# Kernel tuning notes

Measured on AMD Instinct MI355X. Metric: run time of the kernel, lower is better.

The kernel has to match this reference:

```python
import jax, jax.numpy as jnp
import numpy as np

B, T, D, NH, V, L = 2, 1024, 1024, 16, 32000, 4  # L = blocks * layers_per_block
HD = D // NH
FF = 4 * D


def rmsnorm(x, gamma, beta):
    # matches RMSNorm: mean of squares over last dim (tp pmean is identity on 1 device)
    ms = jnp.mean(jnp.square(x), axis=-1, keepdims=True)
    return (x / jnp.sqrt(ms + 1e-6)) * gamma + beta


def setup_inputs() -> dict:
    key = jax.random.key(0)
    ks = jax.random.split(key, 16)
    s = 0.02
    inp = {
        "tokens": jax.random.randint(ks[0], (B, T), 0, V, dtype=jnp.int32),
        "emb_W": jax.random.normal(ks[1], (V, D), jnp.float32) * s,
        "pos_W": jax.random.normal(ks[2], (T, D), jnp.float32) * s,
        "g1": jnp.ones((L, D), jnp.float32),
        "be1": jnp.zeros((L, D), jnp.float32),
        "Wqkv": jax.random.normal(ks[3], (L, D, 3 * D), jnp.float32) * s,
        "bqkv": jnp.zeros((L, 3 * D), jnp.float32),
        "Wo": jax.random.normal(ks[4], (L, D, D), jnp.float32) * s,
        "bo": jnp.zeros((L, D), jnp.float32),
        "g2": jnp.ones((L, D), jnp.float32),
        "be2": jnp.zeros((L, D), jnp.float32),
        "Wf1": jax.random.normal(ks[5], (L, D, FF), jnp.float32) * s,
        "bf1": jnp.zeros((L, FF), jnp.float32),
        "Wf2": jax.random.normal(ks[6], (L, FF, D), jnp.float32) * s,
        "bf2": jnp.zeros((L, D), jnp.float32),
        "gf": jnp.ones((D,), jnp.float32),
        "bef": jnp.zeros((D,), jnp.float32),
    }
    return inp


def _forward(tokens, emb_W, pos_W, g1, be1, Wqkv, bqkv, Wo, bo, g2, be2,
             Wf1, bf1, Wf2, bf2, gf, bef):
    x = emb_W[tokens] + pos_W[jnp.arange(T)]  # [B, T, D]
    causal = jnp.tril(jnp.ones((T, T), dtype=bool))
    scale = HD ** -0.5
    for i in range(L):
        # attention sub-block
        h = rmsnorm(x, g1[i], be1[i])
        qkv = h @ Wqkv[i] + bqkv[i]
        q, k, v = jnp.split(qkv, 3, axis=-1)
        q = q.reshape(B, T, NH, HD).transpose(0, 2, 1, 3)  # B nh T d
        k = k.reshape(B, T, NH, HD).transpose(0, 2, 1, 3)
        v = v.reshape(B, T, NH, HD).transpose(0, 2, 1, 3)
        att = jnp.einsum('bhqd,bhkd->bhqk', q, k) * scale
        att = jnp.where(causal, att, -jnp.inf)
        att = jax.nn.softmax(att, axis=-1)
        o = jnp.einsum('bhqk,bhkd->bhqd', att, v)
        o = o.transpose(0, 2, 1, 3).reshape(B, T, D)
        x = x + (o @ Wo[i] + bo[i])
        # FFN sub-block (selu, dropout off since train=False)
        h = rmsnorm(x, g2[i], be2[i])
        f = jax.nn.selu(h @ Wf1[i] + bf1[i]) @ Wf2[i] + bf2[i]
        x = x + f
    # tied output head: final RMSNorm then embedding.attend
    x = rmsnorm(x, gf, bef)
    logits = jnp.einsum('btd,vd->btv', x, emb_W)
    return logits


def reference(tokens, emb_W, pos_W, g1, be1, Wqkv, bqkv, Wo, bo, g2, be2,
              Wf1, bf1, Wf2, bf2, gf, bef):
    return _forward(tokens, emb_W, pos_W, g1, be1, Wqkv, bqkv, Wo, bo,
                    g2, be2, Wf1, bf1, Wf2, bf2, gf, bef)
```

## Files before the change

### kernel.cpp

```cpp
#include <hip/hip_runtime.h>

typedef unsigned short u16;
typedef __attribute__((ext_vector_type(8))) short bf16x8;
typedef __attribute__((ext_vector_type(4))) float f32x4;

#define DD 1024
#define TT 1024
#define NHH 16
#define VV 32000
#define FFF 4096
#define LL 4
#define MM 2048
#define TD3 3072

__device__ __forceinline__ u16 f2bfu(float f) {
  unsigned int x = __builtin_bit_cast(unsigned int, f);
  return (u16)((x + 0x7FFFu + ((x >> 16) & 1u)) >> 16);
}

__device__ __forceinline__ void gl16(const u16* g, u16* l) {
  __builtin_amdgcn_global_load_lds((const __attribute__((address_space(1))) void*)g,
                                   (__attribute__((address_space(3))) void*)l, 16, 0, 0);
}

template <int N>
__device__ __forceinline__ void vwait() {
  if constexpr (N == 0) asm volatile("s_waitcnt vmcnt(0)" ::: "memory");
  else if constexpr (N == 4) asm volatile("s_waitcnt vmcnt(4)" ::: "memory");
  else asm volatile("s_waitcnt vmcnt(8)" ::: "memory");
}

__global__ void transpose_cvt_k(const float* __restrict__ in, u16* __restrict__ out,
                                int K, int N) {
  const size_t mat = (size_t)K * N;
  in += (size_t)blockIdx.z * mat;
  out += (size_t)blockIdx.z * mat;
  __shared__ float tile[32][33];
  const int n0 = blockIdx.x << 5, k0 = blockIdx.y << 5;
  const int tx = threadIdx.x, ty = threadIdx.y;
#pragma unroll
  for (int i = 0; i < 32; i += 8) tile[ty + i][tx] = in[(size_t)(k0 + ty + i) * N + n0 + tx];
  __syncthreads();
#pragma unroll
  for (int i = 0; i < 32; i += 8)
    out[(size_t)(n0 + ty + i) * K + k0 + tx] = f2bfu(tile[tx][ty + i]);
}

__global__ void cvt_bf16_k(const float* __restrict__ in, u16* __restrict__ out, long n4) {
  const long i = (long)blockIdx.x * blockDim.x + threadIdx.x;
  if (i >= n4) return;
  const float4 v = ((const float4*)in)[i];
  ushort4 o;
  o.x = f2bfu(v.x); o.y = f2bfu(v.y); o.z = f2bfu(v.z); o.w = f2bfu(v.w);
  ((ushort4*)out)[i] = o;
}

__global__ void embed_k(const int* __restrict__ tok, const float* __restrict__ emb,
                        const float* __restrict__ pos, float* __restrict__ x) {
  const int m = blockIdx.x, tid = threadIdx.x;
  const int t = m & (TT - 1);
  const int id = tok[m];
  const float4 e = ((const float4*)(emb + (size_t)id * DD))[tid];
  const float4 p = ((const float4*)(pos + (size_t)t * DD))[tid];
  float4 r;
  r.x = e.x + p.x; r.y = e.y + p.y; r.z = e.z + p.z; r.w = e.w + p.w;
  ((float4*)(x + (size_t)m * DD))[tid] = r;
}

__global__ void rmsnorm_k(const float* __restrict__ x, const float* __restrict__ g,
                          const float* __restrict__ be, u16* __restrict__ out) {
  const int row = blockIdx.x, tid = threadIdx.x;
  const float4 xv = ((const float4*)(x + (size_t)row * DD))[tid];
  float ss = xv.x * xv.x + xv.y * xv.y + xv.z * xv.z + xv.w * xv.w;
#pragma unroll
  for (int o = 32; o; o >>= 1) ss += __shfl_xor(ss, o);
  __shared__ float sm[4];
  if ((tid & 63) == 0) sm[tid >> 6] = ss;
  __syncthreads();
  const float tot = sm[0] + sm[1] + sm[2] + sm[3];
  const float rs = rsqrtf(tot * (1.f / DD) + 1e-6f);
  const float4 gv = ((const float4*)g)[tid];
  const float4 bv = ((const float4*)be)[tid];
  ushort4 o4;
  o4.x = f2bfu(xv.x * rs * gv.x + bv.x);
  o4.y = f2bfu(xv.y * rs * gv.y + bv.y);
  o4.z = f2bfu(xv.z * rs * gv.z + bv.z);
  o4.w = f2bfu(xv.w * rs * gv.w + bv.w);
  ((ushort4*)(out + (size_t)row * DD))[tid] = o4;
}

template <int NP>
__global__ void addres_rms_k(float* __restrict__ x, const float* __restrict__ pp,
                             const float* __restrict__ bias, const float* __restrict__ g,
                             const float* __restrict__ be, u16* __restrict__ out) {
  const int row = blockIdx.x, tid = threadIdx.x;
  const size_t base = (size_t)row * (DD / 4) + tid;
  float4 s = ((float4*)x)[base];
  const float4 bv = ((const float4*)bias)[tid];
  s.x += bv.x; s.y += bv.y; s.z += bv.z; s.w += bv.w;
#pragma unroll
  for (int p = 0; p < NP; ++p) {
    const float4 pv = ((const float4*)pp)[(size_t)p * (MM * DD / 4) + base];
    s.x += pv.x; s.y += pv.y; s.z += pv.z; s.w += pv.w;
  }
  ((float4*)x)[base] = s;
  float ss = s.x * s.x + s.y * s.y + s.z * s.z + s.w * s.w;
#pragma unroll
  for (int o = 32; o; o >>= 1) ss += __shfl_xor(ss, o);
  __shared__ float sm[4];
  if ((tid & 63) == 0) sm[tid >> 6] = ss;
  __syncthreads();
  const float tot = sm[0] + sm[1] + sm[2] + sm[3];
  const float rs = rsqrtf(tot * (1.f / DD) + 1e-6f);
  const float4 gv = ((const float4*)g)[tid];
  const float4 bev = ((const float4*)be)[tid];
  ushort4 o4;
  o4.x = f2bfu(s.x * rs * gv.x + bev.x);
  o4.y = f2bfu(s.y * rs * gv.y + bev.y);
  o4.z = f2bfu(s.z * rs * gv.z + bev.z);
  o4.w = f2bfu(s.w * rs * gv.w + bev.w);
  ((ushort4*)(out + (size_t)row * DD))[tid] = o4;
}

__global__ void pack_vt_k(const u16* __restrict__ qkv, u16* __restrict__ Vt) {
  const int z = blockIdx.x;
  const int t0 = blockIdx.y << 6;
  const int b = z >> 4, h = z & 15;
  __shared__ u16 tile[64][72];
  const int tid = threadIdx.x;
  for (int c = tid; c < 512; c += 256) {
    const int t = c >> 3, d8 = (c & 7) << 3;
    union { uint4 u; u16 s[8]; } tmp;
    tmp.u = *(const uint4*)(qkv + (long)(b * TT + t0 + t) * TD3 + 2 * DD + h * 64 + d8);
#pragma unroll
    for (int j = 0; j < 8; ++j) tile[d8 + j][t] = tmp.s[j];
  }
  __syncthreads();
  for (int c = tid; c < 512; c += 256) {
    const int d = c >> 3, t8 = (c & 7) << 3;
    *(uint4*)(Vt + ((long)z * 64 + d) * TT + t0 + t8) = *(const uint4*)&tile[d][t8];
  }
}

__global__ __launch_bounds__(256) void flash_k(const u16* __restrict__ qkv,
                                               const u16* __restrict__ Vt,
                                               u16* __restrict__ o) {
  const int z = blockIdx.x;
  const int pair = blockIdx.y;
  const int b = z >> 4, h = z & 15;
  const int tid = threadIdx.x;
  const int lane = tid & 63;
  const int w = tid >> 6;

  __shared__ u16 Qs[64 * 64];
  __shared__ u16 Ks[128 * 64];
  __shared__ u16 Vs[64 * 128];
  __shared__ u16 Ps[64 * 128];

  const u16* qbase = qkv + (size_t)b * TT * TD3;
  const int kcb = (lane >> 4) << 4;

  for (int half = 0; half < 2; ++half) {
    const int qa = half ? (15 - pair) : pair;
    const int q0 = qa << 6;
    const int nkt = (qa >> 1) + 1;

#pragma unroll
    for (int c = 0; c < 2; ++c) {
      const int rbase = c * 32 + w * 8;
      const int row = rbase + (lane >> 3);
      const u16* src = qbase + (long)(q0 + row) * TD3 + h * 64 +
                       ((((lane & 7) << 4) ^ ((row & 7) << 4)) >> 1);
      gl16(src, &Qs[rbase * 64]);
    }

    float m_r[4], l_r[4];
    f32x4 oacc[4];
#pragma unroll
    for (int r = 0; r < 4; ++r) { m_r[r] = -1e30f; l_r[r] = 0.f; }
#pragma unroll
    for (int nd = 0; nd < 4; ++nd) oacc[nd] = (f32x4){0.f, 0.f, 0.f, 0.f};

    for (int kt = 0; kt < nkt; ++kt) {
      const int t0 = kt << 7;
#pragma unroll
      for (int c = 0; c < 4; ++c) {
        const int rbase = c * 32 + w * 8;
        const int row = rbase + (lane >> 3);
        const u16* src = qbase + (long)(t0 + row) * TD3 + DD + h * 64 +
                         ((((lane & 7) << 4) ^ ((row & 7) << 4)) >> 1);
        gl16(src, &Ks[rbase * 64]);
      }
#pragma unroll
      for (int c = 0; c < 4; ++c) {
        const int rbase = c * 16 + w * 4;
        const int d = rbase + (lane >> 4);
        const u16* src = Vt + ((long)(z * 64 + d)) * TT + t0 +
                         ((((lane & 15) << 4) ^ ((d & 7) << 4)) >> 1);
        gl16(src, &Vs[rbase * 128]);
      }
      __syncthreads();

      f32x4 sacc[8];
#pragma unroll
      for (int ni = 0; ni < 8; ++ni) sacc[ni] = (f32x4){0.f, 0.f, 0.f, 0.f};
      const int qrow = (w << 4) + (lane & 15);
#pragma unroll
      for (int ks = 0; ks < 2; ++ks) {
        const bf16x8 aq = *(const bf16x8*)&Qs[qrow * 64 + (((ks * 64 + kcb) ^ ((qrow & 7) << 4)) >> 1)];
#pragma unroll
        for (int ni = 0; ni < 8; ++ni) {
          const int key = (lane & 15) + (ni << 4);
          const bf16x8 bk = *(const bf16x8*)&Ks[key * 64 + (((ks * 64 + kcb) ^ ((key & 7) << 4)) >> 1)];
          sacc[ni] = __builtin_amdgcn_mfma_f32_16x16x32_bf16(aq, bk, sacc[ni], 0, 0, 0);
        }
      }

      float mx[4] = {-1e30f, -1e30f, -1e30f, -1e30f};
      const bool diag = (kt == nkt - 1);
#pragma unroll
      for (int ni = 0; ni < 8; ++ni)
#pragma unroll
        for (int r = 0; r < 4; ++r) {
          float v = sacc[ni][r] * 0.125f;
          if (diag) {
            const int key = t0 + (lane & 15) + (ni << 4);
            const int qq = q0 + (w << 4) + ((lane >> 4) << 2) + r;
            if (key > qq) v = -1e30f;
          }
          sacc[ni][r] = v;
          mx[r] = fmaxf(mx[r], v);
        }
#pragma unroll
      for (int st = 1; st < 16; st <<= 1)
#pragma unroll
        for (int r = 0; r < 4; ++r) mx[r] = fmaxf(mx[r], __shfl_xor(mx[r], st));
      float sc[4], sum[4];
#pragma unroll
      for (int r = 0; r < 4; ++r) {
        const float mn = fmaxf(m_r[r], mx[r]);
        sc[r] = __expf(m_r[r] - mn);
        m_r[r] = mn;
        sum[r] = 0.f;
      }
#pragma unroll
      for (int ni = 0; ni < 8; ++ni)
#pragma unroll
        for (int r = 0; r < 4; ++r) {
          const float e = __expf(sacc[ni][r] - m_r[r]);
          sum[r] += e;
          const int prow = (w << 4) + ((lane >> 4) << 2) + r;
          const int pcol = (lane & 15) + (ni << 4);
          Ps[prow * 128 + (((pcol << 1) ^ ((prow & 7) << 4)) >> 1)] = f2bfu(e);
        }
#pragma unroll
      for (int st = 1; st < 16; st <<= 1)
#pragma unroll
        for (int r = 0; r < 4; ++r) sum[r] += __shfl_xor(sum[r], st);
#pragma unroll
      for (int r = 0; r < 4; ++r) l_r[r] = l_r[r] * sc[r] + sum[r];
#pragma unroll
      for (int nd = 0; nd < 4; ++nd)
#pragma unroll
        for (int r = 0; r < 4; ++r) oacc[nd][r] *= sc[r];

#pragma unroll
      for (int ks2 = 0; ks2 < 4; ++ks2) {
        const int prow = (w << 4) + (lane & 15);
        const bf16x8 pa = *(const bf16x8*)&Ps[prow * 128 + (((ks2 * 64 + kcb) ^ ((prow & 7) << 4)) >> 1)];
#pragma unroll
        for (int nd = 0; nd < 4; ++nd) {
          const int dd2 = (lane & 15) + (nd << 4);
          const bf16x8 vb = *(const bf16x8*)&Vs[dd2 * 128 + (((ks2 * 64 + kcb) ^ ((dd2 & 7) << 4)) >> 1)];
          oacc[nd] = __builtin_amdgcn_mfma_f32_16x16x32_bf16(pa, vb, oacc[nd], 0, 0, 0);
        }
      }
      __syncthreads();
    }

    float inv[4];
#pragma unroll
    for (int r = 0; r < 4; ++r) inv[r] = 1.f / l_r[r];
#pragma unroll
    for (int nd = 0; nd < 4; ++nd)
#pragma unroll
      for (int r = 0; r < 4; ++r) {
        const int row = q0 + (w << 4) + ((lane >> 4) << 2) + r;
        const int col = (h << 6) + (lane & 15) + (nd << 4);
        o[(long)(b * TT + row) * DD + col] = f2bfu(oacc[nd][r] * inv[r]);
      }
  }
}

enum { EPI_BF16 = 0, EPI_BF16_BIAS = 1, EPI_SELU = 2, EPI_F32 = 3, EPI_RESID = 4 };

template <int EPI>
__global__ __launch_bounds__(256) void gemm_bt(
    const u16* __restrict__ A, long az1, long az2, int lda,
    const u16* __restrict__ Bt, long bz1, long bz2, int ldb,
    void* __restrict__ C, long cz1, long cz2, int ldc,
    const float* __restrict__ bias, int Nvalid, int K) {
  const int z = blockIdx.z;
  A += (long)(z >> 4) * az1 + (long)(z & 15) * az2;
  Bt += (long)(z >> 4) * bz1 + (long)(z & 15) * bz2;
  const long coff = (long)(z >> 4) * cz1 + (long)(z & 15) * cz2;

  __shared__ u16 ldsA[2][128 * 32];
  __shared__ u16 ldsB[2][128 * 32];

  const int tid = threadIdx.x;
  const int lane = tid & 63;
  const int wave = tid >> 6;
  const int wr = wave >> 1, wc = wave & 1;
  const int m0 = blockIdx.x << 7, n0 = blockIdx.y << 7;

  f32x4 acc[4][4];
#pragma unroll
  for (int i = 0; i < 4; ++i)
#pragma unroll
    for (int j = 0; j < 4; ++j) acc[i][j] = (f32x4){0.f, 0.f, 0.f, 0.f};

  auto STAGE = [&](int buf, int kt) {
    const int k0 = kt << 5;
#pragma unroll
    for (int p = 0; p < 2; ++p) {
      const int c = tid + (p << 8);
      const int row = c >> 2, col = (c & 3) << 3;
      gl16(A + (long)(m0 + row) * lda + k0 + col, &ldsA[buf][c << 3]);
      gl16(Bt + (long)(n0 + row) * ldb + k0 + col, &ldsB[buf][c << 3]);
    }
  };

  const int nk = K >> 5;
  STAGE(0, 0);
  __syncthreads();
  int cur = 0;
  for (int kt = 0; kt < nk; ++kt) {
    if (kt + 1 < nk) STAGE(cur ^ 1, kt + 1);
    const int rb = lane & 15;
    const int kc = (lane >> 4) << 3;
    bf16x8 af[4], bfr[4];
#pragma unroll
    for (int mi = 0; mi < 4; ++mi)
      af[mi] = *(const bf16x8*)&ldsA[cur][(((wr << 6) + (mi << 4) + rb) << 5) + kc];
#pragma unroll
    for (int ni = 0; ni < 4; ++ni)
      bfr[ni] = *(const bf16x8*)&ldsB[cur][(((wc << 6) + (ni << 4) + rb) << 5) + kc];
#pragma unroll
    for (int mi = 0; mi < 4; ++mi)
#pragma unroll
      for (int ni = 0; ni < 4; ++ni)
        acc[mi][ni] = __builtin_amdgcn_mfma_f32_16x16x32_bf16(af[mi], bfr[ni], acc[mi][ni], 0, 0, 0);
    __syncthreads();
    cur ^= 1;
  }

  const int row0 = m0 + (wr << 6) + ((lane >> 4) << 2);
  const int col0 = n0 + (wc << 6) + (lane & 15);
#pragma unroll
  for (int ni = 0; ni < 4; ++ni) {
    const int col = col0 + (ni << 4);
    if (col >= Nvalid) continue;
    float bv = 0.f;
    if (EPI == EPI_BF16_BIAS || EPI == EPI_SELU || EPI == EPI_RESID) bv = bias[col];
#pragma unroll
    for (int mi = 0; mi < 4; ++mi) {
#pragma unroll
      for (int r = 0; r < 4; ++r) {
        const int row = row0 + (mi << 4) + r;
        const long idx = coff + (long)row * ldc + col;
        float v = acc[mi][ni][r] + bv;
        if (EPI == EPI_SELU)
          v = v > 0.f ? 1.0507009873554805f * v : 1.7580993408473766f * (__expf(v) - 1.f);
        if (EPI == EPI_BF16 || EPI == EPI_BF16_BIAS || EPI == EPI_SELU)
          ((u16*)C)[idx] = f2bfu(v);
        else if (EPI == EPI_F32)
          ((float*)C)[idx] = v;
        else
          ((float*)C)[idx] += v;
      }
    }
  }
}

template <int EPI, int KDIM>
__global__ __launch_bounds__(512) void gemm256_k(
    const u16* __restrict__ A, int lda,
    const u16* __restrict__ Bt, int ldb,
    void* __restrict__ C, int ldc,
    const float* __restrict__ bias, int mm) {
  extern __shared__ u16 smem[];
  u16* SA = smem;
  u16* SB = smem + 24576;

  const int nwg = gridDim.x;
  const int q = nwg >> 3, r = nwg & 7;
  const int xcd = blockIdx.x & 7, loc = blockIdx.x >> 3;
  const int wg = (xcd < r) ? (xcd * (q + 1) + loc) : (r * (q + 1) + (xcd - r) * q + loc);
  const int m0 = (wg % mm) << 8;
  const int n0 = (wg / mm) << 8;

  const int tid = threadIdx.x;
  const int lane = tid & 63;
  const int w = tid >> 6;
  const int wr = w >> 2, wc = w & 3;
  const int l = lane & 15, kq = lane >> 4;

  f32x4 acc[8][4];
#pragma unroll
  for (int i = 0; i < 8; ++i)
#pragma unroll
    for (int j = 0; j < 4; ++j) acc[i][j] = (f32x4){0.f, 0.f, 0.f, 0.f};

  auto STAGE = [&](int p, int kt) {
    u16* la = SA + (p << 13);
    u16* lb = SB + (p << 13);
    const int k0 = kt << 5;
#pragma unroll
    for (int hh = 0; hh < 2; ++hh) {
      const int c = tid + (hh << 9);
      const int r2 = c >> 3, sp = c & 7;
      const int s = sp ^ (r2 & 7);
      const int row = r2 + ((s >> 2) << 7);
      const int col = k0 + ((s & 3) << 3);
      gl16(A + (size_t)(m0 + row) * lda + col, la + (c << 3));
      gl16(Bt + (size_t)(n0 + row) * ldb + col, lb + (c << 3));
    }
  };

  constexpr int NK = KDIM >> 5;
  STAGE(0, 0);
  STAGE(1, 1);
  STAGE(2, 2);

  int buf = 0;
#pragma unroll 1
  for (int t = 0; t < NK; ++t) {
    if (t + 2 < NK) vwait<8>();
    else if (t + 1 < NK) vwait<4>();
    else vwait<0>();
    __builtin_amdgcn_s_barrier();
    __builtin_amdgcn_sched_barrier(0);

    const u16* a = SA + (buf << 13);
    const u16* b = SB + (buf << 13);
    auto rdA = [&](int mi) -> bf16x8 {
      const int row = (wr << 7) + (mi << 4) + l;
      const int r2 = row & 127;
      const int sp = (((row >> 7) << 2) + kq) ^ (r2 & 7);
      return *(const bf16x8*)&a[(r2 << 6) + (sp << 3)];
    };
    auto rdB = [&](int ni) -> bf16x8 {
      const int row = (wc << 6) + (ni << 4) + l;
      const int r2 = row & 127;
      const int sp = (((row >> 7) << 2) + kq) ^ (r2 & 7);
      return *(const bf16x8*)&b[(r2 << 6) + (sp << 3)];
    };

    bf16x8 bfr[4], afA[2], afB[2];
    bfr[0] = rdB(0); bfr[1] = rdB(1); bfr[2] = rdB(2); bfr[3] = rdB(3);
    afA[0] = rdA(0); afA[1] = rdA(1);
    __builtin_amdgcn_sched_barrier(0);
    afB[0] = rdA(2); afB[1] = rdA(3);
    __builtin_amdgcn_sched_barrier(0);

    __builtin_amdgcn_s_setprio(1);
#pragma unroll
    for (int ni = 0; ni < 4; ++ni) {
      acc[0][ni] = __builtin_amdgcn_mfma_f32_16x16x32_bf16(afA[0], bfr[ni], acc[0][ni], 0, 0, 0);
      acc[1][ni] = __builtin_amdgcn_mfma_f32_16x16x32_bf16(afA[1], bfr[ni], acc[1][ni], 0, 0, 0);
    }
    __builtin_amdgcn_s_setprio(0);
    __builtin_amdgcn_sched_barrier(0);
    afA[0] = rdA(4); afA[1] = rdA(5);
    __builtin_amdgcn_sched_barrier(0);
    __builtin_amdgcn_s_setprio(1);
#pragma unroll
    for (int ni = 0; ni < 4; ++ni) {
      acc[2][ni] = __builtin_amdgcn_mfma_f32_16x16x32_bf16(afB[0], bfr[ni], acc[2][ni], 0, 0, 0);
      acc[3][ni] = __builtin_amdgcn_mfma_f32_16x16x32_bf16(afB[1], bfr[ni], acc[3][ni], 0, 0, 0);
    }
    __builtin_amdgcn_s_setprio(0);
    __builtin_amdgcn_sched_barrier(0);
    afB[0] = rdA(6); afB[1] = rdA(7);
    __builtin_amdgcn_sched_barrier(0);
    __builtin_amdgcn_s_setprio(1);
#pragma unroll
    for (int ni = 0; ni < 4; ++ni) {
      acc[4][ni] = __builtin_amdgcn_mfma_f32_16x16x32_bf16(afA[0], bfr[ni], acc[4][ni], 0, 0, 0);
      acc[5][ni] = __builtin_amdgcn_mfma_f32_16x16x32_bf16(afA[1], bfr[ni], acc[5][ni], 0, 0, 0);
    }
    __builtin_amdgcn_s_setprio(0);
    __builtin_amdgcn_sched_barrier(0);

    asm volatile("s_waitcnt lgkmcnt(0)" ::: "memory");
    __builtin_amdgcn_sched_barrier(0);
    __builtin_amdgcn_s_barrier();
    __builtin_amdgcn_sched_barrier(0);
    if (t + 3 < NK) STAGE(buf, t + 3);
    __builtin_amdgcn_sched_barrier(0);

    __builtin_amdgcn_s_setprio(1);
#pragma unroll
    for (int ni = 0; ni < 4; ++ni) {
      acc[6][ni] = __builtin_amdgcn_mfma_f32_16x16x32_bf16(afB[0], bfr[ni], acc[6][ni], 0, 0, 0);
      acc[7][ni] = __builtin_amdgcn_mfma_f32_16x16x32_bf16(afB[1], bfr[ni], acc[7][ni], 0, 0, 0);
    }
    __builtin_amdgcn_s_setprio(0);
    buf = (buf == 2) ? 0 : buf + 1;
  }

  const int row0 = m0 + (wr << 7) + ((lane >> 4) << 2);
  const int col0 = n0 + (wc << 6) + (lane & 15);
#pragma unroll
  for (int ni = 0; ni < 4; ++ni) {
    const int col = col0 + (ni << 4);
    float bv = 0.f;
    if (EPI == EPI_BF16_BIAS || EPI == EPI_SELU) bv = bias[col];
#pragma unroll
    for (int mi = 0; mi < 8; ++mi) {
#pragma unroll
      for (int r = 0; r < 4; ++r) {
        const int row = row0 + (mi << 4) + r;
        const long idx = (long)row * ldc + col;
        float v = acc[mi][ni][r] + bv;
        if (EPI == EPI_SELU)
          v = v > 0.f ? 1.0507009873554805f * v : 1.7580993408473766f * (__expf(v) - 1.f);
        if (EPI == EPI_BF16 || EPI == EPI_BF16_BIAS || EPI == EPI_SELU)
          ((u16*)C)[idx] = f2bfu(v);
        else
          ((float*)C)[idx] = v;
      }
    }
  }
}

extern "C" void kernel_launch(void* const* d_in, const int* in_sizes, int n_in,
                              void* d_out, int out_size, void* d_ws, size_t ws_size,
                              hipStream_t stream) {
  const int* tokens = (const int*)d_in[0];
  const float* emb_W = (const float*)d_in[1];
  const float* pos_W = (const float*)d_in[2];
  const float* g1 = (const float*)d_in[3];
  const float* be1 = (const float*)d_in[4];
  const float* Wqkv = (const float*)d_in[5];
  const float* bqkv = (const float*)d_in[6];
  const float* Wo = (const float*)d_in[7];
  const float* bo = (const float*)d_in[8];
  const float* g2 = (const float*)d_in[9];
  const float* be2 = (const float*)d_in[10];
  const float* Wf1 = (const float*)d_in[11];
  const float* bf1 = (const float*)d_in[12];
  const float* Wf2 = (const float*)d_in[13];
  const float* bf2 = (const float*)d_in[14];
  const float* gf = (const float*)d_in[15];
  const float* bef = (const float*)d_in[16];

  char* w = (char*)d_ws;
  auto alloc = [&](size_t bytes) {
    char* p = w;
    w += (bytes + 255) & ~(size_t)255;
    return p;
  };
  u16* WqkvT = (u16*)alloc((size_t)LL * TD3 * DD * 2);
  u16* WoT   = (u16*)alloc((size_t)LL * DD * DD * 2);
  u16* Wf1T  = (u16*)alloc((size_t)LL * FFF * DD * 2);
  u16* Wf2T  = (u16*)alloc((size_t)LL * DD * FFF * 2);
  u16* embB  = (u16*)alloc((size_t)VV * DD * 2);
  float* x   = (float*)alloc((size_t)MM * DD * 4);
  u16* h     = (u16*)alloc((size_t)MM * DD * 2);
  u16* qkv   = (u16*)alloc((size_t)MM * TD3 * 2);
  u16* Vt    = (u16*)alloc((size_t)32 * 64 * TT * 2);
  u16* o     = (u16*)alloc((size_t)MM * DD * 2);
  u16* h1    = (u16*)alloc((size_t)MM * FFF * 2);
  float* pp  = (float*)alloc((size_t)4 * MM * DD * 4);

  bool big =
      hipFuncSetAttribute((const void*)&gemm256_k<EPI_F32, 1024>,
                          hipFuncAttributeMaxDynamicSharedMemorySize, 98304) == hipSuccess;

  dim3 tb(32, 8);
  transpose_cvt_k<<<dim3(TD3 / 32, DD / 32, LL), tb, 0, stream>>>(Wqkv, WqkvT, DD, TD3);
  transpose_cvt_k<<<dim3(DD / 32, DD / 32, LL), tb, 0, stream>>>(Wo, WoT, DD, DD);
  transpose_cvt_k<<<dim3(FFF / 32, DD / 32, LL), tb, 0, stream>>>(Wf1, Wf1T, DD, FFF);
  transpose_cvt_k<<<dim3(DD / 32, FFF / 32, LL), tb, 0, stream>>>(Wf2, Wf2T, FFF, DD);
  cvt_bf16_k<<<(VV * DD / 4) / 256, 256, 0, stream>>>(emb_W, embB, (long)VV * DD / 4);
  embed_k<<<MM, 256, 0, stream>>>(tokens, emb_W, pos_W, x);
  rmsnorm_k<<<MM, 256, 0, stream>>>(x, g1, be1, h);

  for (int i = 0; i < LL; ++i) {
    gemm_bt<EPI_BF16_BIAS><<<dim3(16, 24, 1), 256, 0, stream>>>(
        h, 0, 0, DD, WqkvT + (size_t)i * TD3 * DD, 0, 0, DD,
        qkv, 0, 0, TD3, bqkv + i * TD3, TD3, DD);
    pack_vt_k<<<dim3(32, 16), 256, 0, stream>>>(qkv, Vt);
    flash_k<<<dim3(32, 8), 256, 0, stream>>>(qkv, Vt, o);
    gemm_bt<EPI_F32><<<dim3(16, 8, 2), 256, 0, stream>>>(
        o, 0, 512, DD, WoT + (size_t)i * DD * DD, 0, 512, DD,
        pp, 0, (long)MM * DD, DD, nullptr, DD, 512);
    addres_rms_k<2><<<MM, 256, 0, stream>>>(x, pp, bo + i * DD, g2 + i * DD, be2 + i * DD, h);
    gemm_bt<EPI_SELU><<<dim3(16, 32, 1), 256, 0, stream>>>(
        h, 0, 0, DD, Wf1T + (size_t)i * FFF * DD, 0, 0, DD,
        h1, 0, 0, FFF, bf1 + i * FFF, FFF, DD);
    gemm_bt<EPI_F32><<<dim3(16, 8, 4), 256, 0, stream>>>(
        h1, 0, 1024, FFF, Wf2T + (size_t)i * DD * FFF, 0, 1024, FFF,
        pp, 0, (long)MM * DD, DD, nullptr, DD, 1024);
    const bool last = (i == LL - 1);
    addres_rms_k<4><<<MM, 256, 0, stream>>>(
        x, pp, bf2 + i * DD,
        last ? gf : g1 + (i + 1) * DD, last ? bef : be1 + (i + 1) * DD, h);
  }

  if (big) {
    gemm256_k<EPI_F32, 1024><<<1000, 512, 98304, stream>>>(
        h, DD, embB, DD, (float*)d_out, VV, nullptr, 8);
  } else {
    gemm_bt<EPI_F32><<<dim3(16, 250, 1), 256, 0, stream>>>(
        h, 0, 0, DD, embB, 0, 0, DD,
        (float*)d_out, 0, 0, VV, nullptr, VV, DD);
  }
}
```

Measured before the change: 993.8 us.

## Add triple-buffered layer GEMM, restructure logits GEMM loop and LDS-staged epilogue

Result: slower. 1.064 ms (+7.1%).

```diff
diff --git a/kernel.cpp b/kernel.cpp
--- a/kernel.cpp
+++ b/kernel.cpp
@@ -383,12 +383,116 @@
   }
 }
 
-template <int EPI, int KDIM>
+template <int EPI>
+__global__ __launch_bounds__(256) void gemm_bt3(
+    const u16* __restrict__ A, long az1, long az2, int lda,
+    const u16* __restrict__ Bt, long bz1, long bz2, int ldb,
+    void* __restrict__ C, long cz1, long cz2, int ldc,
+    const float* __restrict__ bias, int Nvalid, int K) {
+  const int z = blockIdx.z;
+  A += (long)(z >> 4) * az1 + (long)(z & 15) * az2;
+  Bt += (long)(z >> 4) * bz1 + (long)(z & 15) * bz2;
+  const long coff = (long)(z >> 4) * cz1 + (long)(z & 15) * cz2;
+
+  __shared__ u16 ldsA[3][128 * 32];
+  __shared__ u16 ldsB[3][128 * 32];
+
+  const int tid = threadIdx.x;
+  const int lane = tid & 63;
+  const int wave = tid >> 6;
+  const int wr = wave >> 1, wc = wave & 1;
+  const int m0 = blockIdx.x << 7, n0 = blockIdx.y << 7;
+
+  f32x4 acc[4][4];
+#pragma unroll
+  for (int i = 0; i < 4; ++i)
+#pragma unroll
+    for (int j = 0; j < 4; ++j) acc[i][j] = (f32x4){0.f, 0.f, 0.f, 0.f};
+
+  auto STAGE = [&](int buf, int kt) {
+    const int k0 = kt << 5;
+#pragma unroll
+    for (int p = 0; p < 2; ++p) {
+      const int c = tid + (p << 8);
+      const int row = c >> 2, col = (c & 3) << 3;
+      gl16(A + (long)(m0 + row) * lda + k0 + col, &ldsA[buf][c << 3]);
+      gl16(Bt + (long)(n0 + row) * ldb + k0 + col, &ldsB[buf][c << 3]);
+    }
+  };
+
+  const int nk = K >> 5;
+  STAGE(0, 0);
+  STAGE(1, 1);
+
+  const int rb = lane & 15;
+  const int kc = (lane >> 4) << 3;
+  int cur = 0, stg = 2;
+#pragma unroll 1
+  for (int kt = 0; kt < nk; ++kt) {
+    if (kt + 1 < nk) vwait<4>();
+    else vwait<0>();
+    __builtin_amdgcn_s_barrier();
+    __builtin_amdgcn_sched_barrier(0);
+
+    bf16x8 af[4], bfr[4];
+#pragma unroll
+    for (int mi = 0; mi < 4; ++mi)
+      af[mi] = *(const bf16x8*)&ldsA[cur][(((wr << 6) + (mi << 4) + rb) << 5) + kc];
+#pragma unroll
+    for (int ni = 0; ni < 4; ++ni)
+      bfr[ni] = *(const bf16x8*)&ldsB[cur][(((wc << 6) + (ni << 4) + rb) << 5) + kc];
+    asm volatile("s_waitcnt lgkmcnt(0)" ::: "memory");
+    __builtin_amdgcn_sched_barrier(0);
+    __builtin_amdgcn_s_barrier();
+    __builtin_amdgcn_sched_barrier(0);
+    if (kt + 2 < nk) STAGE(stg, kt + 2);
+    __builtin_amdgcn_sched_barrier(0);
+
+    __builtin_amdgcn_s_setprio(1);
+#pragma unroll
+    for (int mi = 0; mi < 4; ++mi)
+#pragma unroll
+      for (int ni = 0; ni < 4; ++ni)
+        acc[mi][ni] = __builtin_amdgcn_mfma_f32_16x16x32_bf16(af[mi], bfr[ni], acc[mi][ni], 0, 0, 0);
+    __builtin_amdgcn_s_setprio(0);
+
+    cur = (cur == 2) ? 0 : cur + 1;
+    stg = (stg == 2) ? 0 : stg + 1;
+  }
+
+  const int row0 = m0 + (wr << 6) + ((lane >> 4) << 2);
+  const int col0 = n0 + (wc << 6) + (lane & 15);
+#pragma unroll
+  for (int ni = 0; ni < 4; ++ni) {
+    const int col = col0 + (ni << 4);
+    if (col >= Nvalid) continue;
+    float bv = 0.f;
+    if (EPI == EPI_BF16_BIAS || EPI == EPI_SELU || EPI == EPI_RESID) bv = bias[col];
+#pragma unroll
+    for (int mi = 0; mi < 4; ++mi) {
+#pragma unroll
+      for (int r = 0; r < 4; ++r) {
+        const int row = row0 + (mi << 4) + r;
+        const long idx = coff + (long)row * ldc + col;
+        float v = acc[mi][ni][r] + bv;
+        if (EPI == EPI_SELU)
+          v = v > 0.f ? 1.0507009873554805f * v : 1.7580993408473766f * (__expf(v) - 1.f);
+        if (EPI == EPI_BF16 || EPI == EPI_BF16_BIAS || EPI == EPI_SELU)
+          ((u16*)C)[idx] = f2bfu(v);
+        else if (EPI == EPI_F32)
+          ((float*)C)[idx] = v;
+        else
+          ((float*)C)[idx] += v;
+      }
+    }
+  }
+}
+
+template <int KDIM>
 __global__ __launch_bounds__(512) void gemm256_k(
     const u16* __restrict__ A, int lda,
     const u16* __restrict__ Bt, int ldb,
-    void* __restrict__ C, int ldc,
-    const float* __restrict__ bias, int mm) {
+    float* __restrict__ C, int ldc, int mm) {
   extern __shared__ u16 smem[];
   u16* SA = smem;
   u16* SB = smem + 24576;
@@ -457,80 +561,47 @@
       return *(const bf16x8*)&b[(r2 << 6) + (sp << 3)];
     };
 
-    bf16x8 bfr[4], afA[2], afB[2];
-    bfr[0] = rdB(0); bfr[1] = rdB(1); bfr[2] = rdB(2); bfr[3] = rdB(3);
-    afA[0] = rdA(0); afA[1] = rdA(1);
-    __builtin_amdgcn_sched_barrier(0);
-    afB[0] = rdA(2); afB[1] = rdA(3);
+    bf16x8 af[8], bfr[4];
+#pragma unroll
+    for (int ni = 0; ni < 4; ++ni) bfr[ni] = rdB(ni);
+#pragma unroll
+    for (int mi = 0; mi < 8; ++mi) af[mi] = rdA(mi);
+    asm volatile("s_waitcnt lgkmcnt(0)" ::: "memory");
+    __builtin_amdgcn_sched_barrier(0);
+    __builtin_amdgcn_s_barrier();
+    __builtin_amdgcn_sched_barrier(0);
+    if (t + 3 < NK) STAGE(buf, t + 3);
     __builtin_amdgcn_sched_barrier(0);
 
     __builtin_amdgcn_s_setprio(1);
 #pragma unroll
-    for (int ni = 0; ni < 4; ++ni) {
-      acc[0][ni] = __builtin_amdgcn_mfma_f32_16x16x32_bf16(afA[0], bfr[ni], acc[0][ni], 0, 0, 0);
-      acc[1][ni] = __builtin_amdgcn_mfma_f32_16x16x32_bf16(afA[1], bfr[ni], acc[1][ni], 0, 0, 0);
-    }
-    __builtin_amdgcn_s_setprio(0);
-    __builtin_amdgcn_sched_barrier(0);
-    afA[0] = rdA(4); afA[1] = rdA(5);
-    __builtin_amdgcn_sched_barrier(0);
-    __builtin_amdgcn_s_setprio(1);
-#pragma unroll
-    for (int ni = 0; ni < 4; ++ni) {
-      acc[2][ni] = __builtin_amdgcn_mfma_f32_16x16x32_bf16(afB[0], bfr[ni], acc[2][ni], 0, 0, 0);
-      acc[3][ni] = __builtin_amdgcn_mfma_f32_16x16x32_bf16(afB[1], bfr[ni], acc[3][ni], 0, 0, 0);
-    }
-    __builtin_amdgcn_s_setprio(0);
-    __builtin_amdgcn_sched_barrier(0);
-    afB[0] = rdA(6); afB[1] = rdA(7);
-    __builtin_amdgcn_sched_barrier(0);
-    __builtin_amdgcn_s_setprio(1);
-#pragma unroll
-    for (int ni = 0; ni < 4; ++ni) {
-      acc[4][ni] = __builtin_amdgcn_mfma_f32_16x16x32_bf16(afA[0], bfr[ni], acc[4][ni], 0, 0, 0);
-      acc[5][ni] = __builtin_amdgcn_mfma_f32_16x16x32_bf16(afA[1], bfr[ni], acc[5][ni], 0, 0, 0);
-    }
-    __builtin_amdgcn_s_setprio(0);
-    __builtin_amdgcn_sched_barrier(0);
-
-    asm volatile("s_waitcnt lgkmcnt(0)" ::: "memory");
-    __builtin_amdgcn_sched_barrier(0);
-    __builtin_amdgcn_s_barrier();
-    __builtin_amdgcn_sched_barrier(0);
-    if (t + 3 < NK) STAGE(buf, t + 3);
-    __builtin_amdgcn_sched_barrier(0);
-
-    __builtin_amdgcn_s_setprio(1);
-#pragma unroll
-    for (int ni = 0; ni < 4; ++ni) {
-      acc[6][ni] = __builtin_amdgcn_mfma_f32_16x16x32_bf16(afB[0], bfr[ni], acc[6][ni], 0, 0, 0);
-      acc[7][ni] = __builtin_amdgcn_mfma_f32_16x16x32_bf16(afB[1], bfr[ni], acc[7][ni], 0, 0, 0);
-    }
+    for (int mi = 0; mi < 8; ++mi)
+#pragma unroll
+      for (int ni = 0; ni < 4; ++ni)
+        acc[mi][ni] = __builtin_amdgcn_mfma_f32_16x16x32_bf16(af[mi], bfr[ni], acc[mi][ni], 0, 0, 0);
     __builtin_amdgcn_s_setprio(0);
     buf = (buf == 2) ? 0 : buf + 1;
   }
 
-  const int row0 = m0 + (wr << 7) + ((lane >> 4) << 2);
-  const int col0 = n0 + (wc << 6) + (lane & 15);
-#pragma unroll
-  for (int ni = 0; ni < 4; ++ni) {
-    const int col = col0 + (ni << 4);
-    float bv = 0.f;
-    if (EPI == EPI_BF16_BIAS || EPI == EPI_SELU) bv = bias[col];
-#pragma unroll
-    for (int mi = 0; mi < 8; ++mi) {
-#pragma unroll
-      for (int r = 0; r < 4; ++r) {
-        const int row = row0 + (mi << 4) + r;
-        const long idx = (long)row * ldc + col;
-        float v = acc[mi][ni][r] + bv;
-        if (EPI == EPI_SELU)
-          v = v > 0.f ? 1.0507009873554805f * v : 1.7580993408473766f * (__expf(v) - 1.f);
-        if (EPI == EPI_BF16 || EPI == EPI_BF16_BIAS || EPI == EPI_SELU)
-          ((u16*)C)[idx] = f2bfu(v);
-        else
-          ((float*)C)[idx] = v;
-      }
+  float* lf = (float*)smem + (size_t)w * 1088;
+#pragma unroll 1
+  for (int mi = 0; mi < 8; ++mi) {
+    asm volatile("s_waitcnt lgkmcnt(0)" ::: "memory");
+    __builtin_amdgcn_sched_barrier(0);
+#pragma unroll
+    for (int ni = 0; ni < 4; ++ni)
+#pragma unroll
+      for (int rr = 0; rr < 4; ++rr)
+        lf[((kq << 2) + rr) * 68 + (ni << 4) + l] = acc[mi][ni][rr];
+    asm volatile("s_waitcnt lgkmcnt(0)" ::: "memory");
+    __builtin_amdgcn_sched_barrier(0);
+#pragma unroll
+    for (int p = 0; p < 4; ++p) {
+      const int rl = (p << 2) + kq;
+      const f32x4 v = *(const f32x4*)&lf[rl * 68 + (l << 2)];
+      const int row = m0 + (wr << 7) + (mi << 4) + rl;
+      const int col = n0 + (wc << 6) + (l << 2);
+      *(f32x4*)(C + (size_t)row * ldc + col) = v;
     }
   }
 }
@@ -576,7 +647,7 @@
   float* pp  = (float*)alloc((size_t)4 * MM * DD * 4);
 
   bool big =
-      hipFuncSetAttribute((const void*)&gemm256_k<EPI_F32, 1024>,
+      hipFuncSetAttribute((const void*)&gemm256_k<1024>,
                           hipFuncAttributeMaxDynamicSharedMemorySize, 98304) == hipSuccess;
 
   dim3 tb(32, 8);
@@ -589,19 +660,19 @@
   rmsnorm_k<<<MM, 256, 0, stream>>>(x, g1, be1, h);
 
   for (int i = 0; i < LL; ++i) {
-    gemm_bt<EPI_BF16_BIAS><<<dim3(16, 24, 1), 256, 0, stream>>>(
+    gemm_bt3<EPI_BF16_BIAS><<<dim3(16, 24, 1), 256, 0, stream>>>(
         h, 0, 0, DD, WqkvT + (size_t)i * TD3 * DD, 0, 0, DD,
         qkv, 0, 0, TD3, bqkv + i * TD3, TD3, DD);
     pack_vt_k<<<dim3(32, 16), 256, 0, stream>>>(qkv, Vt);
     flash_k<<<dim3(32, 8), 256, 0, stream>>>(qkv, Vt, o);
-    gemm_bt<EPI_F32><<<dim3(16, 8, 2), 256, 0, stream>>>(
+    gemm_bt3<EPI_F32><<<dim3(16, 8, 2), 256, 0, stream>>>(
         o, 0, 512, DD, WoT + (size_t)i * DD * DD, 0, 512, DD,
         pp, 0, (long)MM * DD, DD, nullptr, DD, 512);
     addres_rms_k<2><<<MM, 256, 0, stream>>>(x, pp, bo + i * DD, g2 + i * DD, be2 + i * DD, h);
-    gemm_bt<EPI_SELU><<<dim3(16, 32, 1), 256, 0, stream>>>(
+    gemm_bt3<EPI_SELU><<<dim3(16, 32, 1), 256, 0, stream>>>(
         h, 0, 0, DD, Wf1T + (size_t)i * FFF * DD, 0, 0, DD,
         h1, 0, 0, FFF, bf1 + i * FFF, FFF, DD);
-    gemm_bt<EPI_F32><<<dim3(16, 8, 4), 256, 0, stream>>>(
+    gemm_bt3<EPI_F32><<<dim3(16, 8, 4), 256, 0, stream>>>(
         h1, 0, 1024, FFF, Wf2T + (size_t)i * DD * FFF, 0, 1024, FFF,
         pp, 0, (long)MM * DD, DD, nullptr, DD, 1024);
     const bool last = (i == LL - 1);
@@ -611,8 +682,8 @@
   }
 
   if (big) {
-    gemm256_k<EPI_F32, 1024><<<1000, 512, 98304, stream>>>(
-        h, DD, embB, DD, (float*)d_out, VV, nullptr, 8);
+    gemm256_k<1024><<<1000, 512, 98304, stream>>>(
+        h, DD, embB, DD, (float*)d_out, VV, 8);
   } else {
     gemm_bt<EPI_F32><<<dim3(16, 250, 1), 256, 0, stream>>>(
         h, 0, 0, DD, embB, 0, 0, DD,
```
